# Performance work log

Hardware: AMD Instinct MI355X
Metric: run time of the kernel (lower is better)

Reference implementation:

```python
import jax, jax.numpy as jnp
import numpy as np

D = 128; H = 8; L = 3; FF = 512; HID = 512
B = 512; N = 20
KD = D // H
CLIP = 10.0


def _bn(x, g, b):
    # BatchNorm1d over flattened (B*n, D), training-mode batch stats, affine
    m = jnp.mean(x, axis=(0, 1)); v = jnp.var(x, axis=(0, 1))
    return (x - m) * jax.lax.rsqrt(v + 1e-5) * g + b


def _mha(x, Wq, Wk, Wv, Wo):
    q = jnp.einsum('bnd,hdk->hbnk', x, Wq)
    k = jnp.einsum('bnd,hdk->hbnk', x, Wk)
    v = jnp.einsum('bnd,hdk->hbnk', x, Wv)
    a = jax.nn.softmax(jnp.einsum('hbnk,hbmk->hbnm', q, k) / np.float32(np.sqrt(KD)), axis=-1)
    h = jnp.einsum('hbnm,hbmk->hbnk', a, v)
    return jnp.einsum('hbnk,hkd->bnd', h, Wo)


def _encode(x, Wq, Wk, Wv, Wo, g1, b1, fW1, fb1, fW2, fb2, g2, b2):
    for l in range(L):
        x = _bn(x + _mha(x, Wq[l], Wk[l], Wv[l], Wo[l]), g1[l], b1[l])
        f = jnp.maximum(x @ fW1[l] + fb1[l], 0.0) @ fW2[l] + fb2[l]
        x = _bn(x + f, g2[l], b2[l])
    return x


def _forward(coords, Wi, bi, W_ph, enc_Wq, enc_Wk, enc_Wv, enc_Wo, enc_g1, enc_b1,
             enc_ffW1, enc_ffb1, enc_ffW2, enc_ffb2, enc_g2, enc_b2,
             W_node, W_fixed, W_step, W_out, Wc1, bc1, Wc2, bc2):
    Bs, Ns, _ = coords.shape
    bid = jnp.arange(Bs)
    x = coords @ Wi + bi                                   # (B,N,D) initial embeddings
    crd = coords
    node_idx = jnp.broadcast_to(jnp.arange(Ns)[None, :], (Bs, Ns))
    # state is re-made each step, so step context is always the placeholder
    step_ctx = jnp.broadcast_to(W_ph[None, :], (Bs, 2 * D))
    ctx_q = step_ctx @ W_step                              # (B,D), constant across steps
    log_ps = []; irs = []; vals = []; tours = []
    first = prev = cur = None
    for i in range(Ns):  # sequential decode loop (shapes shrink each step)
        n = Ns - i
        E = _encode(x, enc_Wq, enc_Wk, enc_Wv, enc_Wo, enc_g1, enc_b1,
                    enc_ffW1, enc_ffb1, enc_ffW2, enc_ffb2, enc_g2, enc_b2)  # (B,n,D)
        g_mean = jnp.mean(E, axis=1)                       # (B,D)
        q = g_mean @ W_fixed + ctx_q                       # (B,D)
        gK, gV, lK = jnp.split(E @ W_node, 3, axis=-1)     # each (B,n,D)
        qh = q.reshape(Bs, H, KD)
        a = jax.nn.softmax(jnp.einsum('bhk,bnhk->bhn', qh, gK.reshape(Bs, n, H, KD)) / np.float32(np.sqrt(KD)), axis=-1)
        glimpse = jnp.einsum('bhn,bnhk->bhk', a, gV.reshape(Bs, n, H, KD)).reshape(Bs, D) @ W_out
        logits = jnp.tanh(jnp.einsum('bd,bnd->bn', glimpse, lK) / np.float32(np.sqrt(D))) * CLIP
        log_p = jax.nn.log_softmax(logits, axis=-1)        # mask all-False (fresh state)
        sel = jnp.argmax(log_p, axis=1)                    # greedy decode
        log_ps.append(log_p[bid, sel])
        cur = crd[bid, sel]
        if i == 0:
            first = cur
            irs.append(jnp.zeros((Bs,), coords.dtype))
        else:
            irs.append(-jnp.sqrt(jnp.sum((cur - prev) ** 2, axis=1)))
        h = jnp.maximum(jnp.concatenate([g_mean, step_ctx], axis=1) @ Wc1 + bc1, 0.0)
        vals.append((h @ Wc2 + bc2)[:, 0])
        tours.append(node_idx[bid, sel])
        if i < Ns - 1:
            sel_mask = (jnp.arange(n)[None, :] == sel[:, None]).astype(jnp.int32)
            keep = jnp.argsort(sel_mask, axis=1)[:, : n - 1]  # stable: drops selected, keeps order
            crd = jnp.take_along_axis(crd, keep[:, :, None], axis=1)
            x = jnp.take_along_axis(x, keep[:, :, None], axis=1)
            node_idx = jnp.take_along_axis(node_idx, keep, axis=1)
        prev = cur
    reward_final = -jnp.sqrt(jnp.sum((first - cur) ** 2, axis=1))
    tours = jnp.stack(tours, axis=1)                        # (B,N) int
    d = jnp.take_along_axis(coords, tours[:, :, None], axis=1)
    cost = jnp.sum(jnp.linalg.norm(d[:, 1:] - d[:, :-1], axis=2), axis=1) + jnp.linalg.norm(d[:, 0] - d[:, -1], axis=1)
    return (jnp.stack(log_ps, 1), jnp.stack(irs, 1), jnp.stack(vals, 1), cost, reward_final, tours)


def setup_inputs():
    key = jax.random.key(0)
    ks = jax.random.split(key, 16)
    def nrm(k, shp, scale=0.02):
        return jax.random.normal(k, shp, dtype=jnp.float32) * scale
    return {
        'coords': jax.random.uniform(ks[0], (B, N, 2), dtype=jnp.float32),
        'Wi': nrm(ks[1], (2, D), 0.5),
        'bi': jnp.zeros((D,), jnp.float32),
        'W_ph': jax.random.uniform(ks[2], (2 * D,), jnp.float32, -1.0, 1.0),
        'enc_Wq': nrm(ks[3], (L, H, D, KD)),
        'enc_Wk': nrm(ks[4], (L, H, D, KD)),
        'enc_Wv': nrm(ks[5], (L, H, D, KD)),
        'enc_Wo': nrm(ks[6], (L, H, KD, D)),
        'enc_g1': jnp.ones((L, D), jnp.float32),
        'enc_b1': jnp.zeros((L, D), jnp.float32),
        'enc_ffW1': nrm(ks[7], (L, D, FF)),
        'enc_ffb1': jnp.zeros((L, FF), jnp.float32),
        'enc_ffW2': nrm(ks[8], (L, FF, D)),
        'enc_ffb2': jnp.zeros((L, D), jnp.float32),
        'enc_g2': jnp.ones((L, D), jnp.float32),
        'enc_b2': jnp.zeros((L, D), jnp.float32),
        'W_node': nrm(ks[9], (D, 3 * D)),
        'W_fixed': nrm(ks[10], (D, D)),
        'W_step': nrm(ks[11], (2 * D, D)),
        'W_out': nrm(ks[12], (D, D)),
        'Wc1': nrm(ks[13], (3 * D, HID)),
        'bc1': jnp.zeros((HID,), jnp.float32),
        'Wc2': nrm(ks[14], (HID, 1)),
        'bc2': jnp.zeros((1,), jnp.float32),
    }


def reference(coords, Wi, bi, W_ph, enc_Wq, enc_Wk, enc_Wv, enc_Wo, enc_g1, enc_b1,
              enc_ffW1, enc_ffb1, enc_ffW2, enc_ffb2, enc_g2, enc_b2,
              W_node, W_fixed, W_step, W_out, Wc1, bc1, Wc2, bc2):
    return _forward(coords, Wi, bi, W_ph, enc_Wq, enc_Wk, enc_Wv, enc_Wo, enc_g1, enc_b1,
                    enc_ffW1, enc_ffb1, enc_ffW2, enc_ffb2, enc_g2, enc_b2,
                    W_node, W_fixed, W_step, W_out, Wc1, bc1, Wc2, bc2)
```

## Files before the change

### kernel.cpp

```cpp
#include <hip/hip_runtime.h>
#include <cmath>

namespace {
constexpr int Hc = 8, FFc = 512, HIDc = 512;
}

struct Params {
  const float *coords, *Wi, *bi, *W_ph;
  const float *Wq, *Wk, *Wv, *Wo, *g1, *b1, *fW1, *fb1, *fW2, *fb2, *g2, *b2;
  const float *W_node, *W_fixed, *W_step, *W_out, *Wc1, *bc1, *Wc2, *bc2;
  float* out;
};

__device__ __align__(16) float g_bn[120 * 8 * 256];
__device__ __align__(16) float g_x[512 * 2560];
__device__ __align__(16) float g_t[512 * 2560];
__device__ __align__(16) float g_h[512 * 2560];
__device__ __align__(16) float g_dec[512 * 7680];
__device__ __align__(16) float g_qv[512 * 128];
__device__ float g_val[512];
__device__ __align__(16) float g_crd[512 * 40];
__device__ int   g_idx[512 * 20];
__device__ float g_state[512 * 8];
__device__ __align__(16) float g_ctxq[128];
__device__ __align__(16) float g_cctx[512];
__device__ __align__(16) float g_Wqp[3 * 16384];
__device__ __align__(16) float g_Wkp[3 * 16384];
__device__ __align__(16) float g_Wvp[3 * 16384];
__device__ __align__(16) float g_Wop[3 * 16384];
__device__ __align__(16) float g_W1q[3 * 65536];
__device__ __align__(16) float g_W2q[3 * 65536];
__device__ __align__(16) float g_Wnp[49152];
__device__ __align__(16) float g_Wfp[16384];
__device__ __align__(16) float g_Woup[16384];
__device__ __align__(16) float g_Wc1p[65536];

#define DOT4(a, b) ((a).x*(b).x + (a).y*(b).y + (a).z*(b).z + (a).w*(b).w)

__device__ __forceinline__ void bn_coef(int slot, const float* g, const float* bb, float cnt,
                                        float* s_scale, float* s_shift, int tid) {
  if (tid < 128) {
    float sm = 0.f, sq = 0.f;
#pragma unroll
    for (int r = 0; r < 8; r++) {
      const float* s = &g_bn[(slot * 8 + r) * 256];
      sm += s[tid]; sq += s[128 + tid];
    }
    float m_ = sm / cnt;
    float v_ = sq / cnt - m_ * m_;
    float rs = rsqrtf(v_ + 1e-5f);
    float sc = rs * g[tid];
    s_scale[tid] = sc;
    s_shift[tid] = bb[tid] - m_ * sc;
  }
}

__global__ __launch_bounds__(256) void kinit(Params p) {
  const int tid = threadIdx.x, b = blockIdx.x;
  const int gid = b * 256 + tid, GS = 512 * 256;
  for (int i = gid; i < 120 * 8 * 256; i += GS) g_bn[i] = 0.f;
  if (gid < 512) g_val[gid] = 0.f;
  for (int e = tid; e < 2560; e += 256) {
    int i = e >> 7, d = e & 127;
    float cx = p.coords[b * 40 + 2 * i], cy = p.coords[b * 40 + 2 * i + 1];
    g_x[b * 2560 + e] = cx * p.Wi[d] + cy * p.Wi[128 + d] + p.bi[d];
  }
  if (tid < 40) g_crd[b * 40 + tid] = p.coords[b * 40 + tid];
  if (tid < 20) g_idx[b * 20 + tid] = tid;
  if (tid < 8) g_state[b * 8 + tid] = 0.f;
  if (b == 0) {
    if (tid < 128) {
      float a = 0.f;
      for (int j = 0; j < 256; j++) a += p.W_ph[j] * p.W_step[j * 128 + tid];
      g_ctxq[tid] = a;
    }
    for (int jj = tid; jj < 512; jj += 256) {
      float a = p.bc1[jj];
      for (int e = 0; e < 256; e++) a += p.W_ph[e] * p.Wc1[(128 + e) * 512 + jj];
      g_cctx[jj] = a;
    }
  }
  for (int e = gid; e < 3 * 16384; e += GS) {
    int sub = e & 3, rest = e >> 2;
    int j = rest & 127, rest2 = rest >> 7, d4 = rest2 & 31, l = rest2 >> 5;
    int d = d4 * 4 + sub;
    int src = l * 16384 + (j >> 4) * 2048 + d * 16 + (j & 15);
    g_Wqp[e] = p.Wq[src]; g_Wkp[e] = p.Wk[src]; g_Wvp[e] = p.Wv[src];
    int c = d;
    g_Wop[e] = p.Wo[l * 16384 + (c >> 4) * 2048 + (c & 15) * 128 + j];
  }
  for (int e = gid; e < 3 * 65536; e += GS) {
    int sub = e & 3, f = (e >> 2) & 16383, l = e >> 16;
    int cg = f & 63, c = (f >> 6) & 7, k4 = f >> 9;
    g_W1q[e] = p.fW1[l * 65536 + (k4 * 4 + sub) * 512 + cg * 8 + c];
  }
  for (int e = gid; e < 3 * 65536; e += GS) {
    int sub = e & 3, f = (e >> 2) & 16383, l = e >> 16;
    int cg = f & 31, c = (f >> 5) & 3, k4 = f >> 7;
    g_W2q[e] = p.fW2[l * 65536 + (k4 * 4 + sub) * 128 + cg * 4 + c];
  }
  for (int e = gid; e < 49152; e += GS) {
    int sub = e & 3, rest = e >> 2;
    int col = rest % 384, e4 = rest / 384;
    g_Wnp[e] = p.W_node[(e4 * 4 + sub) * 384 + col];
  }
  for (int e = gid; e < 16384; e += GS) {
    int sub = e & 3, rest = e >> 2;
    int j = rest & 127, e4 = rest >> 7;
    g_Wfp[e] = p.W_fixed[(e4 * 4 + sub) * 128 + j];
    g_Woup[e] = p.W_out[(e4 * 4 + sub) * 128 + j];
  }
  for (int e = gid; e < 65536; e += GS) {
    int sub = e & 3, rest = e >> 2;
    int jj = rest & 511, e4 = rest >> 9;
    g_Wc1p[e] = p.Wc1[(e4 * 4 + sub) * 512 + jj];
  }
}

__global__ __launch_bounds__(256, 4) void ka1(Params p, int step, int l) {
  const int tid = threadIdx.x, b = blockIdx.x, hb = blockIdx.y;
  const int n = 20 - step;
  const int jc = tid & 63, rg = tid >> 6;
  __shared__ __align__(16) float s_t[2560];
  __shared__ __align__(16) float s_q[1280];
  __shared__ float s_kT[1280];
  __shared__ __align__(16) float s_v[1280];
  __shared__ float s_att[1600];
  __shared__ __align__(16) float s_scale[128], s_shift[128];

  if (l > 0)
    bn_coef(step * 6 + (l - 1) * 2 + 1, p.g2 + (l - 1) * 128, p.b2 + (l - 1) * 128,
            (float)(512 * n), s_scale, s_shift, tid);
  __syncthreads();
  const float4* src4 = (const float4*)((l == 0 ? g_x : g_t) + b * 2560);
  float4* st4 = (float4*)s_t;
  for (int e4 = tid; e4 < n * 32; e4 += 256) {
    float4 x = src4[e4];
    if (l > 0) {
      float4 sc = ((const float4*)s_scale)[e4 & 31];
      float4 sh = ((const float4*)s_shift)[e4 & 31];
      x.x = x.x * sc.x + sh.x; x.y = x.y * sc.y + sh.y;
      x.z = x.z * sc.z + sh.z; x.w = x.w * sc.w + sh.w;
    }
    st4[e4] = x;
  }
  __syncthreads();
  {
    const int j = hb * 64 + jc;
    const float4* wq4 = (const float4*)g_Wqp + l * 4096 + j;
    const float4* wk4 = (const float4*)g_Wkp + l * 4096 + j;
    const float4* wv4 = (const float4*)g_Wvp + l * 4096 + j;
    float aq[5], ak[5], av[5];
#pragma unroll
    for (int r = 0; r < 5; r++) { aq[r] = 0.f; ak[r] = 0.f; av[r] = 0.f; }
    float4 bq = wq4[0], bk = wk4[0], bv = wv4[0];
#pragma unroll 2
    for (int d4 = 0; d4 < 32; d4++) {
      const int dn = (d4 + 1) & 31;
      float4 nq = wq4[dn * 128], nk = wk4[dn * 128], nv = wv4[dn * 128];
#pragma unroll
      for (int r = 0; r < 5; r++) {
        int i = rg + 4 * r;
        if (i < n) {
          float4 x = st4[i * 32 + d4];
          aq[r] += DOT4(x, bq); ak[r] += DOT4(x, bk); av[r] += DOT4(x, bv);
        }
      }
      bq = nq; bk = nk; bv = nv;
    }
#pragma unroll
    for (int r = 0; r < 5; r++) {
      int i = rg + 4 * r;
      if (i < n) {
        s_q[i * 64 + jc] = aq[r];
        s_kT[jc * 20 + i] = ak[r];
        s_v[i * 64 + jc] = av[r];
      }
    }
  }
  __syncthreads();
  const int nn = n * n;
  for (int e = tid; e < 4 * nn; e += 256) {
    int hl = e / nn, rem = e % nn, i = rem / n, m = rem % n;
    float dacc = 0.f;
#pragma unroll
    for (int k2 = 0; k2 < 16; k2++)
      dacc += s_q[i * 64 + hl * 16 + k2] * s_kT[(hl * 16 + k2) * 20 + m];
    s_att[hl * 400 + i * 20 + m] = dacc * 0.25f;
  }
  __syncthreads();
  for (int r = tid; r < 4 * n; r += 256) {
    int hl = r / n, i = r % n;
    float* row = s_att + hl * 400 + i * 20;
    float mx = row[0];
    for (int m = 1; m < n; m++) mx = fmaxf(mx, row[m]);
    float s = 0.f;
    for (int m = 0; m < n; m++) { float ev = __expf(row[m] - mx); row[m] = ev; s += ev; }
    float inv = 1.f / s;
    for (int m = 0; m < n; m++) row[m] *= inv;
  }
  __syncthreads();
  for (int e = tid; e < 4 * n * 16; e += 256) {
    int hl = e / (n * 16), rem = e % (n * 16), i = rem >> 4, k2 = rem & 15;
    const float* arow = s_att + hl * 400 + i * 20;
    float acc = 0.f;
    for (int m = 0; m < n; m++) acc += arow[m] * s_v[m * 64 + hl * 16 + k2];
    g_h[b * 2560 + i * 128 + hb * 64 + hl * 16 + k2] = acc;
  }
}

__global__ __launch_bounds__(256, 4) void ka2(Params p, int step, int l) {
  const int tid = threadIdx.x, b = blockIdx.x, s = blockIdx.y;
  const int n = 20 - step;
  const int jcol = tid & 127, rhalf = tid >> 7;
  __shared__ __align__(16) float s_h[2560];
  __shared__ __align__(16) float s_x[2560];
  __shared__ __align__(16) float s_scale[128], s_shift[128];
  __shared__ float s_sm[128], s_sq[128];

  if (l > 0)
    bn_coef(step * 6 + (l - 1) * 2 + 1, p.g2 + (l - 1) * 128, p.b2 + (l - 1) * 128,
            (float)(512 * n), s_scale, s_shift, tid);
  __syncthreads();
  const float4* src4 = (const float4*)((l == 0 ? g_x : g_t) + b * 2560);
  const float4* gh4 = (const float4*)(g_h + b * 2560);
  float4* sh4 = (float4*)s_h;
  float4* sx4 = (float4*)s_x;
  for (int e4 = tid; e4 < n * 32; e4 += 256) {
    int i = e4 >> 5;
    if (((i ^ s) & 1) == 0) {
      sh4[e4] = gh4[e4];
      float4 x = src4[e4];
      if (l > 0) {
        float4 sc = ((const float4*)s_scale)[e4 & 31];
        float4 sf = ((const float4*)s_shift)[e4 & 31];
        x.x = x.x * sc.x + sf.x; x.y = x.y * sc.y + sf.y;
        x.z = x.z * sc.z + sf.z; x.w = x.w * sc.w + sf.w;
      }
      sx4[e4] = x;
    }
  }
  __syncthreads();
  float acc[5];
#pragma unroll
  for (int r = 0; r < 5; r++) {
    int i = s + 2 * (rhalf + 2 * r);
    acc[r] = (i < n) ? s_x[i * 128 + jcol] : 0.f;
  }
  const float4* wo4 = (const float4*)g_Wop + l * 4096 + jcol;
  float4 wb0 = wo4[0], wb1 = wo4[128];
#pragma unroll 2
  for (int c4 = 0; c4 < 32; c4++) {
    float4 wn = wo4[((c4 + 2) & 31) * 128];
#pragma unroll
    for (int r = 0; r < 5; r++) {
      int i = s + 2 * (rhalf + 2 * r);
      if (i < n) { float4 h = sh4[i * 32 + c4]; acc[r] += DOT4(h, wb0); }
    }
    wb0 = wb1; wb1 = wn;
  }
  float sm = 0.f, sq = 0.f;
#pragma unroll
  for (int r = 0; r < 5; r++) {
    int i = s + 2 * (rhalf + 2 * r);
    if (i < n) { g_t[b * 2560 + i * 128 + jcol] = acc[r]; sm += acc[r]; sq += acc[r] * acc[r]; }
  }
  __syncthreads();
  if (rhalf == 1) { s_sm[jcol] = sm; s_sq[jcol] = sq; }
  __syncthreads();
  if (rhalf == 0) {
    float* slot = &g_bn[((step * 6 + l * 2) * 8 + ((b * 2 + s) & 7)) * 256];
    atomicAdd(&slot[jcol], sm + s_sm[jcol]);
    atomicAdd(&slot[128 + jcol], sq + s_sq[jcol]);
  }
}

__global__ __launch_bounds__(256, 3) void kff(Params p, int step, int l) {
  const int tid = threadIdx.x, bx = blockIdx.x;
  const int n = 20 - step;
  const int r0 = bx * 16;
  __shared__ __align__(16) float s_x[16 * 128];
  __shared__ __align__(16) float s_hid[16 * 512];
  __shared__ __align__(16) float s_scale[128], s_shift[128];
  __shared__ float s_bn[8 * 128 * 2];

  bn_coef(step * 6 + l * 2, p.g1 + l * 128, p.b1 + l * 128, (float)(512 * n), s_scale, s_shift, tid);
  __syncthreads();
  {
    float4* sx4 = (float4*)s_x;
    for (int e4 = tid; e4 < 16 * 32; e4 += 256) {
      int row = e4 >> 5, d4 = e4 & 31;
      int r = r0 + row, b = r / n, i = r - b * n;
      float4 x = *(const float4*)(g_t + b * 2560 + i * 128 + d4 * 4);
      float4 sc = ((const float4*)s_scale)[d4];
      float4 sf = ((const float4*)s_shift)[d4];
      x.x = x.x * sc.x + sf.x; x.y = x.y * sc.y + sf.y;
      x.z = x.z * sc.z + sf.z; x.w = x.w * sc.w + sf.w;
      sx4[e4] = x;
    }
  }
  __syncthreads();
  {
    const int cg = tid & 63, rg = tid >> 6;
    float acc[4][8];
#pragma unroll
    for (int rr = 0; rr < 4; rr++)
#pragma unroll
      for (int c = 0; c < 8; c++) acc[rr][c] = 0.f;
    const float4* w1 = (const float4*)g_W1q + l * 16384 + cg;
    const float4* xx = (const float4*)s_x + rg * 4 * 32;
    float4 wb[8];
#pragma unroll
    for (int c = 0; c < 8; c++) wb[c] = w1[c * 64];
#pragma unroll 2
    for (int k4 = 0; k4 < 32; k4++) {
      float4 wn[8];
      const int kn = (k4 + 1) & 31;
#pragma unroll
      for (int c = 0; c < 8; c++) wn[c] = w1[(kn * 8 + c) * 64];
      float4 xr0 = xx[k4], xr1 = xx[32 + k4], xr2 = xx[64 + k4], xr3 = xx[96 + k4];
#pragma unroll
      for (int c = 0; c < 8; c++) {
        acc[0][c] += DOT4(xr0, wb[c]); acc[1][c] += DOT4(xr1, wb[c]);
        acc[2][c] += DOT4(xr2, wb[c]); acc[3][c] += DOT4(xr3, wb[c]);
      }
#pragma unroll
      for (int c = 0; c < 8; c++) wb[c] = wn[c];
    }
    float4 b1a = *(const float4*)(p.fb1 + l * FFc + cg * 8);
    float4 b1b = *(const float4*)(p.fb1 + l * FFc + cg * 8 + 4);
#pragma unroll
    for (int rr = 0; rr < 4; rr++) {
      int row = rg * 4 + rr;
      float4 u0, u1;
      u0.x = fmaxf(acc[rr][0] + b1a.x, 0.f); u0.y = fmaxf(acc[rr][1] + b1a.y, 0.f);
      u0.z = fmaxf(acc[rr][2] + b1a.z, 0.f); u0.w = fmaxf(acc[rr][3] + b1a.w, 0.f);
      u1.x = fmaxf(acc[rr][4] + b1b.x, 0.f); u1.y = fmaxf(acc[rr][5] + b1b.y, 0.f);
      u1.z = fmaxf(acc[rr][6] + b1b.z, 0.f); u1.w = fmaxf(acc[rr][7] + b1b.w, 0.f);
      *(float4*)&s_hid[row * 512 + cg * 8] = u0;
      *(float4*)&s_hid[row * 512 + cg * 8 + 4] = u1;
    }
  }
  __syncthreads();
  {
    const int cg = tid & 31, rg = tid >> 5;
    float acc0[4], acc1[4];
#pragma unroll
    for (int c = 0; c < 4; c++) { acc0[c] = 0.f; acc1[c] = 0.f; }
    const float4* w2 = (const float4*)g_W2q + l * 16384 + cg;
    const float4* hh = (const float4*)s_hid + rg * 2 * 128;
    float4 wb[8];
#pragma unroll
    for (int c = 0; c < 8; c++) wb[c] = w2[c * 32];
#pragma unroll 2
    for (int k4 = 0; k4 < 128; k4 += 2) {
      float4 wn[8];
      const int kn = (k4 + 2) & 127;
#pragma unroll
      for (int c = 0; c < 8; c++) wn[c] = w2[(kn * 4 + c) * 32];
      float4 h0 = hh[k4], h1 = hh[128 + k4], h2 = hh[k4 + 1], h3 = hh[129 + k4];
#pragma unroll
      for (int c = 0; c < 4; c++) {
        acc0[c] += DOT4(h0, wb[c]); acc0[c] += DOT4(h2, wb[4 + c]);
        acc1[c] += DOT4(h1, wb[c]); acc1[c] += DOT4(h3, wb[4 + c]);
      }
#pragma unroll
      for (int c = 0; c < 8; c++) wb[c] = wn[c];
    }
    float4 f2 = *(const float4*)(p.fb2 + l * 128 + cg * 4);
#pragma unroll
    for (int rr = 0; rr < 2; rr++) {
      int row = rg * 2 + rr;
      int r = r0 + row, b = r / n, i = r - b * n;
      float4 xr = ((const float4*)s_x)[row * 32 + cg];
      float4 u;
      u.x = xr.x + (rr ? acc1[0] : acc0[0]) + f2.x;
      u.y = xr.y + (rr ? acc1[1] : acc0[1]) + f2.y;
      u.z = xr.z + (rr ? acc1[2] : acc0[2]) + f2.z;
      u.w = xr.w + (rr ? acc1[3] : acc0[3]) + f2.w;
      *(float4*)(g_t + b * 2560 + i * 128 + cg * 4) = u;
      if (rr == 0) {
        s_bn[(rg * 128 + cg * 4 + 0) * 2] = u.x; s_bn[(rg * 128 + cg * 4 + 0) * 2 + 1] = u.x * u.x;
        s_bn[(rg * 128 + cg * 4 + 1) * 2] = u.y; s_bn[(rg * 128 + cg * 4 + 1) * 2 + 1] = u.y * u.y;
        s_bn[(rg * 128 + cg * 4 + 2) * 2] = u.z; s_bn[(rg * 128 + cg * 4 + 2) * 2 + 1] = u.z * u.z;
        s_bn[(rg * 128 + cg * 4 + 3) * 2] = u.w; s_bn[(rg * 128 + cg * 4 + 3) * 2 + 1] = u.w * u.w;
      } else {
        s_bn[(rg * 128 + cg * 4 + 0) * 2] += u.x; s_bn[(rg * 128 + cg * 4 + 0) * 2 + 1] += u.x * u.x;
        s_bn[(rg * 128 + cg * 4 + 1) * 2] += u.y; s_bn[(rg * 128 + cg * 4 + 1) * 2 + 1] += u.y * u.y;
        s_bn[(rg * 128 + cg * 4 + 2) * 2] += u.z; s_bn[(rg * 128 + cg * 4 + 2) * 2 + 1] += u.z * u.z;
        s_bn[(rg * 128 + cg * 4 + 3) * 2] += u.w; s_bn[(rg * 128 + cg * 4 + 3) * 2 + 1] += u.w * u.w;
      }
    }
  }
  __syncthreads();
  if (tid < 128) {
    float sm = 0.f, sq = 0.f;
#pragma unroll
    for (int rg = 0; rg < 8; rg++) { sm += s_bn[(rg * 128 + tid) * 2]; sq += s_bn[(rg * 128 + tid) * 2 + 1]; }
    float* slot = &g_bn[((step * 6 + l * 2 + 1) * 8 + (bx & 7)) * 256];
    atomicAdd(&slot[tid], sm);
    atomicAdd(&slot[128 + tid], sq);
  }
}

__global__ __launch_bounds__(256, 4) void kd1(Params p, int step) {
  const int tid = threadIdx.x, b = blockIdx.x, bc = blockIdx.y;
  const int n = 20 - step;
  const int cb = tid & 63, rg = tid >> 6;
  __shared__ __align__(16) float s_t[2560];
  __shared__ __align__(16) float s_scale[128], s_shift[128];
  __shared__ __align__(16) float s_gmean[128];
  __shared__ float s_red[256];

  bn_coef(step * 6 + 5, p.g2 + 2 * 128, p.b2 + 2 * 128, (float)(512 * n), s_scale, s_shift, tid);
  __syncthreads();
  const float4* src4 = (const float4*)(g_t + b * 2560);
  float4* st4 = (float4*)s_t;
  for (int e4 = tid; e4 < n * 32; e4 += 256) {
    float4 x = src4[e4];
    float4 sc = ((const float4*)s_scale)[e4 & 31];
    float4 sf = ((const float4*)s_shift)[e4 & 31];
    x.x = x.x * sc.x + sf.x; x.y = x.y * sc.y + sf.y;
    x.z = x.z * sc.z + sf.z; x.w = x.w * sc.w + sf.w;
    st4[e4] = x;
  }
  __syncthreads();
  if (tid < 128) {
    float ssum = 0.f;
    for (int i2 = 0; i2 < n; i2++) ssum += s_t[i2 * 128 + tid];
    s_gmean[tid] = ssum / (float)n;
  }
  __syncthreads();
  {
    float acc[3][5];
#pragma unroll
    for (int cc = 0; cc < 3; cc++)
#pragma unroll
      for (int r = 0; r < 5; r++) acc[cc][r] = 0.f;
    const float4* wn4 = (const float4*)g_Wnp + bc * 192 + cb;
    float4 b0 = wn4[0], b1 = wn4[64], b2 = wn4[128];
#pragma unroll 2
    for (int d4 = 0; d4 < 32; d4++) {
      const int dn = (d4 + 1) & 31;
      float4 n0 = wn4[dn * 384], n1 = wn4[dn * 384 + 64], n2 = wn4[dn * 384 + 128];
#pragma unroll
      for (int r = 0; r < 5; r++) {
        int i = rg + 4 * r;
        if (i < n) {
          float4 x = st4[i * 32 + d4];
          acc[0][r] += DOT4(x, b0); acc[1][r] += DOT4(x, b1); acc[2][r] += DOT4(x, b2);
        }
      }
      b0 = n0; b1 = n1; b2 = n2;
    }
#pragma unroll
    for (int r = 0; r < 5; r++) {
      int i = rg + 4 * r;
      if (i < n) {
#pragma unroll
        for (int cc = 0; cc < 3; cc++)
          g_dec[b * 7680 + i * 384 + bc * 192 + cb + 64 * cc] = acc[cc][r];
      }
    }
  }
  {
    int jj = bc * 256 + tid;
    float a = g_cctx[jj];
    const float4* wc4 = (const float4*)g_Wc1p + jj;
    const float4* gm4 = (const float4*)s_gmean;
    float4 wb0 = wc4[0], wb1 = wc4[512];
#pragma unroll 2
    for (int e4 = 0; e4 < 32; e4++) {
      float4 wn = wc4[((e4 + 2) & 31) * 512];
      float4 g = gm4[e4]; a += DOT4(g, wb0);
      wb0 = wb1; wb1 = wn;
    }
    s_red[tid] = fmaxf(a, 0.f) * p.Wc2[jj];
  }
  __syncthreads();
#pragma unroll
  for (int sred = 128; sred > 0; sred >>= 1) {
    if (tid < sred) s_red[tid] += s_red[tid + sred];
    __syncthreads();
  }
  if (tid == 0) atomicAdd(&g_val[b], s_red[0]);
  if (bc == 0 && tid < 128) {
    float a = g_ctxq[tid];
    const float4* wf4 = (const float4*)g_Wfp + tid;
    const float4* gm4 = (const float4*)s_gmean;
    float4 wb0 = wf4[0], wb1 = wf4[128];
#pragma unroll 2
    for (int e4 = 0; e4 < 32; e4++) {
      float4 wn = wf4[((e4 + 2) & 31) * 128];
      float4 g = gm4[e4]; a += DOT4(g, wb0);
      wb0 = wb1; wb1 = wn;
    }
    g_qv[b * 128 + tid] = a;
  }
}

__global__ __launch_bounds__(256) void kd2(Params p, int step) {
  const int tid = threadIdx.x, b = blockIdx.x;
  const int n = 20 - step;
  __shared__ __align__(16) float s_dec[7680];
  __shared__ float s_qv[128], s_glq[128];
  __shared__ __align__(16) float s_red[128];
  __shared__ float s_att[160];
  __shared__ float s_logits[20];
  __shared__ int s_sel;

  {
    const float4* src4 = (const float4*)(g_dec + b * 7680);
    float4* sd4 = (float4*)s_dec;
    for (int e4 = tid; e4 < n * 96; e4 += 256) sd4[e4] = src4[e4];
    if (tid < 128) s_qv[tid] = g_qv[b * 128 + tid];
  }
  __syncthreads();
  for (int e = tid; e < Hc * n; e += 256) {
    int hh = e / n, m = e % n;
    float dacc = 0.f;
#pragma unroll
    for (int k2 = 0; k2 < 16; k2++) dacc += s_qv[hh * 16 + k2] * s_dec[m * 384 + hh * 16 + k2];
    s_att[hh * 20 + m] = dacc * 0.25f;
  }
  __syncthreads();
  if (tid < Hc) {
    float* row = s_att + tid * 20;
    float mx = row[0];
    for (int m = 1; m < n; m++) mx = fmaxf(mx, row[m]);
    float s = 0.f;
    for (int m = 0; m < n; m++) { float ev = __expf(row[m] - mx); row[m] = ev; s += ev; }
    float inv = 1.f / s;
    for (int m = 0; m < n; m++) row[m] *= inv;
  }
  __syncthreads();
  if (tid < 128) {
    int hh = tid >> 4;
    const float* arow = s_att + hh * 20;
    float acc = 0.f;
    for (int m = 0; m < n; m++) acc += arow[m] * s_dec[m * 384 + 128 + tid];
    s_red[tid] = acc;
  }
  __syncthreads();
  if (tid < 128) {
    float a = 0.f;
    const float4* wo4 = (const float4*)g_Woup + tid;
    const float4* rr4 = (const float4*)s_red;
    float4 wb0 = wo4[0], wb1 = wo4[128];
#pragma unroll 2
    for (int c4 = 0; c4 < 32; c4++) {
      float4 wn = wo4[((c4 + 2) & 31) * 128];
      float4 r = rr4[c4]; a += DOT4(r, wb0);
      wb0 = wb1; wb1 = wn;
    }
    s_glq[tid] = a;
  }
  __syncthreads();
  if (tid < n) {
    const float* lk = s_dec + tid * 384 + 256;
    float dacc = 0.f;
    for (int d = 0; d < 128; d++) dacc += s_glq[d] * lk[d];
    s_logits[tid] = 10.f * tanhf(dacc / 11.313708498984761f);
  }
  __syncthreads();
  if (tid == 0) {
    float mx = s_logits[0]; int sel = 0;
    for (int i2 = 1; i2 < n; i2++) if (s_logits[i2] > mx) { mx = s_logits[i2]; sel = i2; }
    float s = 0.f;
    for (int i2 = 0; i2 < n; i2++) s += __expf(s_logits[i2] - mx);
    p.out[b * 20 + step] = -logf(s);
    float cx = g_crd[b * 40 + 2 * sel], cy = g_crd[b * 40 + 2 * sel + 1];
    float ir = 0.f;
    if (step > 0) {
      float dx = cx - g_state[b * 8 + 0], dy = cy - g_state[b * 8 + 1];
      float dist = sqrtf(dx * dx + dy * dy);
      ir = -dist;
      g_state[b * 8 + 4] += dist;
    } else { g_state[b * 8 + 2] = cx; g_state[b * 8 + 3] = cy; g_state[b * 8 + 4] = 0.f; }
    p.out[10240 + b * 20 + step] = ir;
    p.out[31744 + b * 20 + step] = (float)g_idx[b * 20 + sel];
    g_state[b * 8 + 0] = cx; g_state[b * 8 + 1] = cy;
    if (step == 19) {
      float dx = g_state[b * 8 + 2] - cx, dy = g_state[b * 8 + 3] - cy;
      float dc = sqrtf(dx * dx + dy * dy);
      p.out[31232 + b] = -dc;
      p.out[30720 + b] = g_state[b * 8 + 4] + dc;
    }
    p.out[20480 + b * 20 + step] = g_val[b] + p.bc2[0];
    g_val[b] = 0.f;
    s_sel = sel;
  }
  __syncthreads();
  if (step < 19) {
    const int sel = s_sel;
    const int movecnt = (n - 1 - sel) * 128;
    float tmp[10]; float crdv = 0.f; int idxv = 0;
#pragma unroll
    for (int r = 0; r < 10; r++) { int e = tid + r * 256; if (e < movecnt) tmp[r] = g_x[b * 2560 + (sel + 1) * 128 + e]; }
    const int mc2 = (n - 1 - sel) * 2;
    if (tid < mc2) crdv = g_crd[b * 40 + (sel + 1) * 2 + tid];
    if (tid < n - 1 - sel) idxv = g_idx[b * 20 + sel + 1 + tid];
    __syncthreads();
#pragma unroll
    for (int r = 0; r < 10; r++) { int e = tid + r * 256; if (e < movecnt) g_x[b * 2560 + sel * 128 + e] = tmp[r]; }
    if (tid < mc2) g_crd[b * 40 + sel * 2 + tid] = crdv;
    if (tid < n - 1 - sel) g_idx[b * 20 + sel + tid] = idxv;
  }
}

extern "C" void kernel_launch(void* const* d_in, const int* in_sizes, int n_in,
                              void* d_out, int out_size, void* d_ws, size_t ws_size,
                              hipStream_t stream) {
  Params p;
  p.coords  = (const float*)d_in[0];
  p.Wi      = (const float*)d_in[1];
  p.bi      = (const float*)d_in[2];
  p.W_ph    = (const float*)d_in[3];
  p.Wq      = (const float*)d_in[4];
  p.Wk      = (const float*)d_in[5];
  p.Wv      = (const float*)d_in[6];
  p.Wo      = (const float*)d_in[7];
  p.g1      = (const float*)d_in[8];
  p.b1      = (const float*)d_in[9];
  p.fW1     = (const float*)d_in[10];
  p.fb1     = (const float*)d_in[11];
  p.fW2     = (const float*)d_in[12];
  p.fb2     = (const float*)d_in[13];
  p.g2      = (const float*)d_in[14];
  p.b2      = (const float*)d_in[15];
  p.W_node  = (const float*)d_in[16];
  p.W_fixed = (const float*)d_in[17];
  p.W_step  = (const float*)d_in[18];
  p.W_out   = (const float*)d_in[19];
  p.Wc1     = (const float*)d_in[20];
  p.bc1     = (const float*)d_in[21];
  p.Wc2     = (const float*)d_in[22];
  p.bc2     = (const float*)d_in[23];
  p.out = (float*)d_out;

  kinit<<<512, 256, 0, stream>>>(p);
  for (int step = 0; step < 20; step++) {
    const int n = 20 - step;
    for (int l = 0; l < 3; l++) {
      ka1<<<dim3(512, 2), 256, 0, stream>>>(p, step, l);
      ka2<<<dim3(512, 2), 256, 0, stream>>>(p, step, l);
      kff<<<dim3(32 * n), 256, 0, stream>>>(p, step, l);
    }
    kd1<<<dim3(512, 2), 256, 0, stream>>>(p, step);
    kd2<<<512, 256, 0, stream>>>(p, step);
  }
}
```

Before: 6.260 ms.

## Stage FFN weight panels into LDS via async global_load_lds triple-buffer ring

Both FFN matmuls in kff now copy 8 KB weight panels straight into a three-slot LDS ring with global_load_lds, waiting with vmcnt and a barrier before each panel is used. This replaces the per-thread register double-buffered weight loads. The aim is to overlap weight fetches with compute and cut register pressure and redundant global reads. In exchange it adds 24 KB of LDS, a barrier per panel, and lowers launch bounds from 3 to 2 blocks per CU, which reduces occupancy.

```diff
diff --git a/kernel.cpp b/kernel.cpp
--- a/kernel.cpp
+++ b/kernel.cpp
@@ -37,6 +37,18 @@
 
 #define DOT4(a, b) ((a).x*(b).x + (a).y*(b).y + (a).z*(b).z + (a).w*(b).w)
 
+__device__ __forceinline__ void gload_lds16(const float* g, float* l) {
+  __builtin_amdgcn_global_load_lds((const __attribute__((address_space(1))) void*)g,
+                                   (__attribute__((address_space(3))) void*)l, 16, 0, 0);
+}
+__device__ __forceinline__ void stage_panel(const float* gsrc, float* ldst, int tid) {
+  const int w = tid >> 6, lane = tid & 63;
+  gload_lds16(gsrc + w * 512 + lane * 4, ldst + w * 512);
+  gload_lds16(gsrc + w * 512 + 256 + lane * 4, ldst + w * 512 + 256);
+}
+#define VM_WAIT2 asm volatile("s_waitcnt vmcnt(2)" ::: "memory")
+#define VM_WAIT0 asm volatile("s_waitcnt vmcnt(0)" ::: "memory")
+
 __device__ __forceinline__ void bn_coef(int slot, const float* g, const float* bb, float cnt,
                                         float* s_scale, float* s_shift, int tid) {
   if (tid < 128) {
@@ -275,12 +287,13 @@
   }
 }
 
-__global__ __launch_bounds__(256, 3) void kff(Params p, int step, int l) {
+__global__ __launch_bounds__(256, 2) void kff(Params p, int step, int l) {
   const int tid = threadIdx.x, bx = blockIdx.x;
   const int n = 20 - step;
   const int r0 = bx * 16;
   __shared__ __align__(16) float s_x[16 * 128];
   __shared__ __align__(16) float s_hid[16 * 512];
+  __shared__ __align__(16) float s_ring[3 * 2048];
   __shared__ __align__(16) float s_scale[128], s_shift[128];
   __shared__ float s_bn[8 * 128 * 2];
 
@@ -307,25 +320,23 @@
     for (int rr = 0; rr < 4; rr++)
 #pragma unroll
       for (int c = 0; c < 8; c++) acc[rr][c] = 0.f;
-    const float4* w1 = (const float4*)g_W1q + l * 16384 + cg;
+    const float* w1f = (const float*)g_W1q + l * 65536;
     const float4* xx = (const float4*)s_x + rg * 4 * 32;
-    float4 wb[8];
-#pragma unroll
-    for (int c = 0; c < 8; c++) wb[c] = w1[c * 64];
-#pragma unroll 2
+    stage_panel(w1f, s_ring, tid);
+    stage_panel(w1f + 2048, s_ring + 2048, tid);
     for (int k4 = 0; k4 < 32; k4++) {
-      float4 wn[8];
-      const int kn = (k4 + 1) & 31;
-#pragma unroll
-      for (int c = 0; c < 8; c++) wn[c] = w1[(kn * 8 + c) * 64];
+      if (k4 < 31) { VM_WAIT2; } else { VM_WAIT0; }
+      __builtin_amdgcn_s_barrier();
+      if (k4 + 2 < 32)
+        stage_panel(w1f + (k4 + 2) * 2048, s_ring + ((k4 + 2) % 3) * 2048, tid);
+      const float4* wp = (const float4*)(s_ring + (k4 % 3) * 2048);
       float4 xr0 = xx[k4], xr1 = xx[32 + k4], xr2 = xx[64 + k4], xr3 = xx[96 + k4];
 #pragma unroll
       for (int c = 0; c < 8; c++) {
-        acc[0][c] += DOT4(xr0, wb[c]); acc[1][c] += DOT4(xr1, wb[c]);
-        acc[2][c] += DOT4(xr2, wb[c]); acc[3][c] += DOT4(xr3, wb[c]);
-      }
-#pragma unroll
-      for (int c = 0; c < 8; c++) wb[c] = wn[c];
+        float4 w = wp[c * 64 + cg];
+        acc[0][c] += DOT4(xr0, w); acc[1][c] += DOT4(xr1, w);
+        acc[2][c] += DOT4(xr2, w); acc[3][c] += DOT4(xr3, w);
+      }
     }
     float4 b1a = *(const float4*)(p.fb1 + l * FFc + cg * 8);
     float4 b1b = *(const float4*)(p.fb1 + l * FFc + cg * 8 + 4);
@@ -347,25 +358,26 @@
     float acc0[4], acc1[4];
 #pragma unroll
     for (int c = 0; c < 4; c++) { acc0[c] = 0.f; acc1[c] = 0.f; }
-    const float4* w2 = (const float4*)g_W2q + l * 16384 + cg;
+    const float* w2f = (const float*)g_W2q + l * 65536;
     const float4* hh = (const float4*)s_hid + rg * 2 * 128;
-    float4 wb[8];
-#pragma unroll
-    for (int c = 0; c < 8; c++) wb[c] = w2[c * 32];
-#pragma unroll 2
-    for (int k4 = 0; k4 < 128; k4 += 2) {
-      float4 wn[8];
-      const int kn = (k4 + 2) & 127;
-#pragma unroll
-      for (int c = 0; c < 8; c++) wn[c] = w2[(kn * 4 + c) * 32];
-      float4 h0 = hh[k4], h1 = hh[128 + k4], h2 = hh[k4 + 1], h3 = hh[129 + k4];
-#pragma unroll
-      for (int c = 0; c < 4; c++) {
-        acc0[c] += DOT4(h0, wb[c]); acc0[c] += DOT4(h2, wb[4 + c]);
-        acc1[c] += DOT4(h1, wb[c]); acc1[c] += DOT4(h3, wb[4 + c]);
-      }
-#pragma unroll
-      for (int c = 0; c < 8; c++) wb[c] = wn[c];
+    stage_panel(w2f, s_ring, tid);
+    stage_panel(w2f + 2048, s_ring + 2048, tid);
+    for (int P = 0; P < 32; P++) {
+      if (P < 31) { VM_WAIT2; } else { VM_WAIT0; }
+      __builtin_amdgcn_s_barrier();
+      if (P + 2 < 32)
+        stage_panel(w2f + (P + 2) * 2048, s_ring + ((P + 2) % 3) * 2048, tid);
+      const float4* wp = (const float4*)(s_ring + (P % 3) * 2048);
+#pragma unroll
+      for (int q = 0; q < 4; q++) {
+        float4 h0 = hh[P * 4 + q], h1 = hh[128 + P * 4 + q];
+#pragma unroll
+        for (int c = 0; c < 4; c++) {
+          float4 w = wp[(q * 4 + c) * 32 + cg];
+          acc0[c] += DOT4(h0, w);
+          acc1[c] += DOT4(h1, w);
+        }
+      }
     }
     float4 f2 = *(const float4*)(p.fb2 + l * 128 + cg * 4);
 #pragma unroll
```

After: 6.890 ms. 10.1% more time.
